# Kernel optimization log

Measured on AMD Instinct MI355X. Metric: run time of the kernel, lower is better.

The kernel has to match this reference:

```python
import jax, jax.numpy as jnp
import numpy as np

EMBED_DIM = 512
NUM_HEADS = 8
HEAD_DIM = EMBED_DIM // NUM_HEADS
LN_EPS = 1e-5


def setup_inputs() -> dict:
    key = jax.random.key(0)
    ks = jax.random.split(key, 7)
    B, S, E = 2, 4096, EMBED_DIM
    s = 1.0 / np.sqrt(E)
    return {
        "x": jax.random.normal(ks[0], (B, S, E), dtype=jnp.float32),
        "qkv_w": jax.random.normal(ks[1], (E, 3 * E), dtype=jnp.float32) * s,
        "qkv_b": jax.random.normal(ks[2], (3 * E,), dtype=jnp.float32) * 0.01,
        "out_w": jax.random.normal(ks[3], (E, E), dtype=jnp.float32) * s,
        "out_b": jax.random.normal(ks[4], (E,), dtype=jnp.float32) * 0.01,
        "ln_g": jnp.ones((E,), dtype=jnp.float32),
        "ln_b": jnp.zeros((E,), dtype=jnp.float32),
    }


def reference(x, qkv_w, qkv_b, out_w, out_b, ln_g, ln_b):
    B, S, E = x.shape
    H, D = NUM_HEADS, HEAD_DIM
    scale = D ** -0.5
    qkv = x @ qkv_w + qkv_b                     # (B, S, 3E)
    qkv = qkv.reshape(B, S, 3, H, D)
    q, k, v = qkv[:, :, 0], qkv[:, :, 1], qkv[:, :, 2]  # (B, S, H, D)
    scores = jnp.einsum("bshd,bthd->bhst", q, k) * scale  # (B, H, S, S)
    probs = jax.nn.softmax(scores, axis=-1)
    ctx = jnp.einsum("bhst,bthd->bshd", probs, v).reshape(B, S, E)
    out = ctx @ out_w + out_b + x               # residual
    mu = out.mean(-1, keepdims=True)
    var = out.var(-1, keepdims=True)
    return (out - mu) * jax.lax.rsqrt(var + LN_EPS) * ln_g + ln_b
```

## Files before the change

### kernel.cpp

```cpp
#include <hip/hip_runtime.h>
#include <stdint.h>

typedef __bf16 bf16x8 __attribute__((ext_vector_type(8)));
typedef float f32x4 __attribute__((ext_vector_type(4)));
typedef float f32x16 __attribute__((ext_vector_type(16)));
typedef float float4v __attribute__((ext_vector_type(4)));
typedef unsigned short u16x4 __attribute__((ext_vector_type(4)));
typedef unsigned short u16x8 __attribute__((ext_vector_type(8)));
typedef unsigned int u32x4v __attribute__((ext_vector_type(4)));

#define DEVI __device__ __forceinline__

static constexpr int Bv = 2, Sv = 4096, Ev = 512, Hv = 8, Dv = 64;
static constexpr int Mv = Bv * Sv;
static constexpr int N3v = 3 * Ev;
static constexpr float QSCALE = 0.125f * 1.4426950408889634f;
static constexpr float C0 = -8.0f;

#if __has_builtin(__builtin_amdgcn_exp2f)
#define EXP2F(x) __builtin_amdgcn_exp2f(x)
#else
#define EXP2F(x) exp2f(x)
#endif

DEVI unsigned short f2bf(float f) {
    unsigned int u = __builtin_bit_cast(unsigned int, f);
    u += 0x7fffu + ((u >> 16) & 1u);
    return (unsigned short)(u >> 16);
}

DEVI float b2f(unsigned short u) {
    return __builtin_bit_cast(float, (unsigned int)u << 16);
}

DEVI unsigned int cvtpk(float lo, float hi) {
    unsigned int r;
    asm("v_cvt_pk_bf16_f32 %0, %1, %2" : "=v"(r) : "v"(lo), "v"(hi));
    return r;
}

DEVI void gload16(const void* src, void* lds) {
    __builtin_amdgcn_global_load_lds(
        (const __attribute__((address_space(1))) unsigned int*)src,
        (__attribute__((address_space(3))) unsigned int*)lds,
        16, 0, 0);
}

__global__ __launch_bounds__(256) void k_convert(const float* __restrict__ in,
                                                 unsigned short* __restrict__ out, int n4) {
    int i = blockIdx.x * 256 + threadIdx.x;
    int stride = gridDim.x * 256;
    for (; i < n4; i += stride) {
        float4v v = ((const float4v*)in)[i];
        u16x4 o;
        o[0] = f2bf(v[0]); o[1] = f2bf(v[1]); o[2] = f2bf(v[2]); o[3] = f2bf(v[3]);
        ((u16x4*)out)[i] = o;
    }
}

__global__ __launch_bounds__(256) void k_tconv(const float* __restrict__ in,
                                               unsigned short* __restrict__ out, int K, int N) {
    __shared__ float lds[32][36];
    int tilesN = N >> 5;
    int tn = blockIdx.x % tilesN, tk = blockIdx.x / tilesN;
    int k0 = tk << 5, n0 = tn << 5;
    int t = threadIdx.x;
    int r = t >> 3, c4 = (t & 7) << 2;
    float4v v = *(const float4v*)(in + (size_t)(k0 + r) * N + n0 + c4);
    *(float4v*)&lds[r][c4] = v;
    __syncthreads();
    int nn = t >> 3, kc = (t & 7) << 2;
    u16x4 o;
#pragma unroll
    for (int j = 0; j < 4; ++j) o[j] = f2bf(lds[kc + j][nn]);
    *(u16x4*)(out + (size_t)(n0 + nn) * K + k0 + kc) = o;
}

template <int EPI>
__global__ __launch_bounds__(256) void k_gemm(
    const unsigned short* __restrict__ A, const unsigned short* __restrict__ Bt,
    int M, int N, int K, const float* __restrict__ bias,
    unsigned short* __restrict__ Qb, unsigned short* __restrict__ Kb,
    unsigned short* __restrict__ Vtb,
    const float* __restrict__ xres, float* __restrict__ outf) {
    __shared__ char smem[32768];
    char* As = smem;
    char* Bs = smem + 16384;
    int nbt = N >> 7;
    int mb = blockIdx.x / nbt, nbi = blockIdx.x % nbt;
    int m0 = mb << 7, n0 = nbi << 7;
    int tid = threadIdx.x, lane = tid & 63, wave = tid >> 6;
    int wr = wave >> 1, wc = wave & 1;

    f32x4 acc[4][4];
    f32x4 zero = {0.f, 0.f, 0.f, 0.f};
#pragma unroll
    for (int a = 0; a < 4; ++a)
#pragma unroll
        for (int b = 0; b < 4; ++b) acc[a][b] = zero;

    for (int kt = 0; kt < K; kt += 64) {
        __syncthreads();
#pragma unroll
        for (int j = 0; j < 4; ++j) {
            int la = (((wave << 2) + j) << 10) + lane * 16;
            int r = la >> 7, cb = la & 127;
            int cbs = cb ^ ((r & 7) << 4);
            gload16((const char*)(A + (size_t)(m0 + r) * K + kt) + cbs,
                    As + (((wave << 2) + j) << 10));
            gload16((const char*)(Bt + (size_t)(n0 + r) * K + kt) + cbs,
                    Bs + (((wave << 2) + j) << 10));
        }
        asm volatile("s_waitcnt vmcnt(0)" ::: "memory");
        __syncthreads();

        bf16x8 af[4][2], bfr[4][2];
#pragma unroll
        for (int rf = 0; rf < 4; ++rf)
#pragma unroll
            for (int c = 0; c < 2; ++c) {
                int row = (wr << 6) + (rf << 4) + (lane & 15);
                int col = (c << 6) + ((lane >> 4) << 4);
                af[rf][c] = *(const bf16x8*)(As + row * 128 + (col ^ ((row & 7) << 4)));
                int rowb = (wc << 6) + (rf << 4) + (lane & 15);
                bfr[rf][c] = *(const bf16x8*)(Bs + rowb * 128 + (col ^ ((rowb & 7) << 4)));
            }
#pragma unroll
        for (int rf = 0; rf < 4; ++rf)
#pragma unroll
            for (int nf = 0; nf < 4; ++nf)
#pragma unroll
                for (int c = 0; c < 2; ++c)
                    acc[rf][nf] = __builtin_amdgcn_mfma_f32_16x16x32_bf16(
                        af[rf][c], bfr[nf][c], acc[rf][nf], 0, 0, 0);
    }

#pragma unroll
    for (int rf = 0; rf < 4; ++rf)
#pragma unroll
        for (int nf = 0; nf < 4; ++nf) {
            int row0 = m0 + (wr << 6) + (rf << 4) + ((lane >> 4) << 2);
            int col = n0 + (wc << 6) + (nf << 4) + (lane & 15);
            float bv = bias[col];
            if (EPI == 0) {
                int reg = col >> 9, hd = col & 511;
                int h = hd >> 6, d = hd & 63;
                int b = row0 >> 12, s0 = row0 & 4095;
                if (reg == 2) {
                    u16x4 o4;
#pragma unroll
                    for (int i = 0; i < 4; ++i) o4[i] = f2bf(acc[rf][nf][i] + bv);
                    *(u16x4*)(Vtb + ((size_t)((b << 3) + h) * 64 + d) * 4096 + s0) = o4;
                } else {
#pragma unroll
                    for (int i = 0; i < 4; ++i) {
                        float v = acc[rf][nf][i] + bv;
                        size_t idx = ((size_t)((b << 3) + h) * Sv + s0 + i) * Dv + d;
                        if (reg == 0) Qb[idx] = f2bf(v * QSCALE);
                        else          Kb[idx] = f2bf(v);
                    }
                }
            } else {
#pragma unroll
                for (int i = 0; i < 4; ++i) {
                    int row = row0 + i;
                    float v = acc[rf][nf][i] + bv + xres[(size_t)row * N + col];
                    outf[(size_t)row * N + col] = v;
                }
            }
        }
}

__global__ __launch_bounds__(256) void k_attn(const unsigned short* __restrict__ Qb,
                                              const unsigned short* __restrict__ Kb,
                                              const unsigned short* __restrict__ Vtb,
                                              unsigned short* __restrict__ po,
                                              float* __restrict__ pl) {
    __shared__ char smem[32768];
    int bid = blockIdx.x;
    int wg = ((bid & 7) << 7) + (bid >> 3);
    int half = wg & 1, qblk = (wg >> 1) & 31, bh = wg >> 6;
    int tid = threadIdx.x, lane = tid & 63, wave = tid >> 6;
    int l31 = lane & 31, hh = lane >> 5;
    int qrow = (qblk << 7) + (wave << 5) + l31;
    int kvbase = half << 11;

    const unsigned short* Kbase = Kb + (size_t)bh * Sv * Dv + (size_t)kvbase * Dv;
    const unsigned short* Vtbase = Vtb + (size_t)bh * Dv * Sv + kvbase;

    bf16x8 qf[4];
#pragma unroll
    for (int tp = 0; tp < 4; ++tp)
        qf[tp] = *(const bf16x8*)(Qb + ((size_t)bh * Sv + qrow) * Dv + (tp << 4) + (hh << 3));

    const char* src[4];
    int strd[4];
    int ldsoff[4];
#pragma unroll
    for (int j = 0; j < 4; ++j) {
        int off = ((wave << 2) + j) << 10;
        int loff = off + lane * 16;
        ldsoff[j] = off;
        if (off < 8192) {
            int r = loff >> 7, cb = loff & 127;
            src[j] = (const char*)(Kbase + (size_t)r * Dv) + (cb ^ ((r & 7) << 4));
            strd[j] = 64 * Dv * 2;
        } else {
            int lo2 = loff - 8192;
            int r = lo2 >> 7, cb = lo2 & 127;
            src[j] = (const char*)(Vtbase + (size_t)r * Sv) + (cb ^ ((r & 7) << 4));
            strd[j] = 64 * 2;
        }
    }

    int koff[2][4], voff[2][2][2];
#pragma unroll
    for (int c = 0; c < 2; ++c) {
        int krow = (c << 5) + l31;
        int ksw = (krow & 7) << 4;
#pragma unroll
        for (int tp = 0; tp < 4; ++tp)
            koff[c][tp] = krow * 128 + (((tp << 5) + (hh << 4)) ^ ksw);
#pragma unroll
        for (int tl = 0; tl < 2; ++tl) {
            int vcb = (c << 6) + (tl << 5) + (hh << 4);
#pragma unroll
            for (int dt = 0; dt < 2; ++dt) {
                int vrow = (dt << 5) + l31;
                voff[c][tl][dt] = vrow * 128 + (vcb ^ ((vrow & 7) << 4));
            }
        }
    }

    f32x16 o[2];
#pragma unroll
    for (int dt = 0; dt < 2; ++dt)
#pragma unroll
        for (int r = 0; r < 16; ++r) o[dt][r] = 0.f;
    float lsum = 0.f;

#pragma unroll
    for (int j = 0; j < 4; ++j) gload16(src[j], smem + ldsoff[j]);
    __syncthreads();

    for (int kt = 0; kt < 32; ++kt) {
        if (kt < 31) {
            int nb = (kt + 1) & 1;
#pragma unroll
            for (int j = 0; j < 4; ++j)
                gload16(src[j] + (size_t)(kt + 1) * strd[j], smem + nb * 16384 + ldsoff[j]);
        }
        char* Ks = smem + (kt & 1) * 16384;
        char* Vs = Ks + 8192;

#pragma unroll
        for (int c = 0; c < 2; ++c) {
            bf16x8 kf[4];
#pragma unroll
            for (int tp = 0; tp < 4; ++tp)
                kf[tp] = *(const bf16x8*)(Ks + koff[c][tp]);
            f32x16 sc;
#pragma unroll
            for (int r = 0; r < 16; ++r) sc[r] = C0;
            __builtin_amdgcn_s_setprio(1);
#pragma unroll
            for (int tp = 0; tp < 4; ++tp)
                sc = __builtin_amdgcn_mfma_f32_32x32x16_bf16(kf[tp], qf[tp], sc, 0, 0, 0);
            __builtin_amdgcn_s_setprio(0);

            float p[16];
#pragma unroll
            for (int r = 0; r < 16; ++r) p[r] = EXP2F(sc[r]);
            float s0 = (p[0] + p[1]) + (p[2] + p[3]);
            float s1 = (p[4] + p[5]) + (p[6] + p[7]);
            float s2 = (p[8] + p[9]) + (p[10] + p[11]);
            float s3 = (p[12] + p[13]) + (p[14] + p[15]);
            lsum += (s0 + s1) + (s2 + s3);

            unsigned int W[8];
#pragma unroll
            for (int i = 0; i < 8; ++i) W[i] = cvtpk(p[2 * i], p[2 * i + 1]);

#pragma unroll
            for (int tl = 0; tl < 2; ++tl) {
                unsigned int a1 = W[4 * tl], b1 = W[4 * tl + 2];
                unsigned int a2 = W[4 * tl + 1], b2 = W[4 * tl + 3];
                asm volatile("v_permlane32_swap_b32 %0, %1" : "+v"(a1), "+v"(b1));
                asm volatile("v_permlane32_swap_b32 %0, %1" : "+v"(a2), "+v"(b2));
                u32x4v uu;
                uu[0] = a1; uu[1] = a2; uu[2] = b1; uu[3] = b2;
                bf16x8 pf = __builtin_bit_cast(bf16x8, uu);
                __builtin_amdgcn_s_setprio(1);
#pragma unroll
                for (int dt = 0; dt < 2; ++dt) {
                    bf16x8 vf = *(const bf16x8*)(Vs + voff[c][tl][dt]);
                    o[dt] = __builtin_amdgcn_mfma_f32_32x32x16_bf16(vf, pf, o[dt], 0, 0, 0);
                }
                __builtin_amdgcn_s_setprio(0);
            }
        }
        __syncthreads();
    }

    lsum += __shfl_xor(lsum, 32, 64);
    if (!hh) pl[((size_t)half * 16 + bh) * Sv + qrow] = lsum;
    size_t obase = (((size_t)half * 16 + bh) * Sv + qrow) * 64;
#pragma unroll
    for (int dt = 0; dt < 2; ++dt)
#pragma unroll
        for (int rp = 0; rp < 8; ++rp) {
            int r = rp << 1;
            int d = (dt << 5) + (r & 3) + ((r >> 2) << 3) + (hh << 2);
            unsigned int w = cvtpk(o[dt][r], o[dt][r + 1]);
            *(unsigned int*)(po + obase + d) = w;
        }
}

__global__ __launch_bounds__(256) void k_merge(const unsigned short* __restrict__ po,
                                               const float* __restrict__ pl,
                                               unsigned short* __restrict__ ctx) {
    int t = blockIdx.x * 256 + threadIdx.x;
    int d8 = t & 7, s = (t >> 3) & 4095, bh = t >> 15;
    int b = bh >> 3, h = bh & 7;
    size_t r0 = ((size_t)bh * 4096 + s) * 64 + (d8 << 3);
    size_t r1 = r0 + (size_t)16 * 4096 * 64;
    u16x8 pa = *(const u16x8*)(po + r0);
    u16x8 pb = *(const u16x8*)(po + r1);
    float inv = 1.f / (pl[(size_t)bh * 4096 + s] + pl[(size_t)16 * 4096 + bh * 4096 + s]);
    u32x4v w;
#pragma unroll
    for (int j = 0; j < 4; ++j) {
        float lo = (b2f(pa[2 * j]) + b2f(pb[2 * j])) * inv;
        float hi = (b2f(pa[2 * j + 1]) + b2f(pb[2 * j + 1])) * inv;
        w[j] = cvtpk(lo, hi);
    }
    *(u32x4v*)(ctx + ((size_t)b * 4096 + s) * 512 + (h << 6) + (d8 << 3)) = w;
}

__global__ __launch_bounds__(256) void k_ln(const float* __restrict__ in,
                                            const float* __restrict__ g,
                                            const float* __restrict__ bta,
                                            float* __restrict__ out) {
    int wave = threadIdx.x >> 6, lane = threadIdx.x & 63;
    size_t row = (size_t)blockIdx.x * 4 + wave;
    const float* p = in + row * 512 + lane * 8;
    float4v v0 = *(const float4v*)p;
    float4v v1 = *(const float4v*)(p + 4);
    float s = 0.f, q = 0.f;
#pragma unroll
    for (int j = 0; j < 4; ++j) {
        s += v0[j] + v1[j];
        q += v0[j] * v0[j] + v1[j] * v1[j];
    }
#pragma unroll
    for (int off = 1; off < 64; off <<= 1) {
        s += __shfl_xor(s, off, 64);
        q += __shfl_xor(q, off, 64);
    }
    float mu = s * (1.f / 512.f);
    float var = q * (1.f / 512.f) - mu * mu;
    float rs = rsqrtf(var + 1e-5f);
    int c = lane * 8;
    float4v o0, o1;
#pragma unroll
    for (int j = 0; j < 4; ++j) {
        o0[j] = (v0[j] - mu) * rs * g[c + j] + bta[c + j];
        o1[j] = (v1[j] - mu) * rs * g[c + 4 + j] + bta[c + 4 + j];
    }
    *(float4v*)(out + row * 512 + c) = o0;
    *(float4v*)(out + row * 512 + c + 4) = o1;
}

extern "C" void kernel_launch(void* const* d_in, const int* in_sizes, int n_in,
                              void* d_out, int out_size, void* d_ws, size_t ws_size,
                              hipStream_t stream) {
    const float* x     = (const float*)d_in[0];
    const float* qkv_w = (const float*)d_in[1];
    const float* qkv_b = (const float*)d_in[2];
    const float* out_w = (const float*)d_in[3];
    const float* out_b = (const float*)d_in[4];
    const float* ln_g  = (const float*)d_in[5];
    const float* ln_b  = (const float*)d_in[6];
    float* out = (float*)d_out;
    char* ws = (char*)d_ws;

    unsigned short* xb    = (unsigned short*)(ws);
    unsigned short* wqkvT = (unsigned short*)(ws + 8388608);
    unsigned short* owT   = (unsigned short*)(ws + 9961472);
    unsigned short* Qb    = (unsigned short*)(ws + 10485760);
    unsigned short* Kb    = (unsigned short*)(ws + 18874368);
    unsigned short* Vtb   = (unsigned short*)(ws + 27262976);
    unsigned short* ctxb  = (unsigned short*)(ws + 35651584);
    unsigned short* po    = (unsigned short*)(ws + 44040192);
    float* tmp            = (float*)(ws + 44040192);
    float* pl             = (float*)(ws + 60817408);

    k_convert<<<2048, 256, 0, stream>>>(x, xb, Mv * Ev / 4);
    k_tconv<<<(512 / 32) * (1536 / 32), 256, 0, stream>>>(qkv_w, wqkvT, 512, 1536);
    k_tconv<<<(512 / 32) * (512 / 32), 256, 0, stream>>>(out_w, owT, 512, 512);
    k_gemm<0><<<(Mv / 128) * (N3v / 128), 256, 0, stream>>>(
        xb, wqkvT, Mv, N3v, Ev, qkv_b, Qb, Kb, Vtb, nullptr, nullptr);
    k_attn<<<1024, 256, 0, stream>>>(Qb, Kb, Vtb, po, pl);
    k_merge<<<2048, 256, 0, stream>>>(po, pl, ctxb);
    k_gemm<1><<<(Mv / 128) * (Ev / 128), 256, 0, stream>>>(
        ctxb, owT, Mv, Ev, Ev, out_b, nullptr, nullptr, nullptr, x, tmp);
    k_ln<<<Mv / 4, 256, 0, stream>>>(tmp, ln_g, ln_b, out);
}
```

Before: 160.8 us.

## Process two query sub-tiles per wave in attention to reuse K/V fragments

Each wave now handles 64 query rows (two 32-row sub-tiles) instead of 32, so every K and V fragment read from LDS feeds twice as many MFMAs. The K/V tile staging cost per query row is halved and the grid is halved to 512 workgroups. In exchange, register pressure roughly doubles for accumulators and Q fragments, which may lower occupancy, and fewer blocks means worse load balance across the 256 CUs.

```diff
diff --git a/kernel.cpp b/kernel.cpp
--- a/kernel.cpp
+++ b/kernel.cpp
@@ -178,20 +178,23 @@
                                               float* __restrict__ pl) {
     __shared__ char smem[32768];
     int bid = blockIdx.x;
-    int wg = ((bid & 7) << 7) + (bid >> 3);
-    int half = wg & 1, qblk = (wg >> 1) & 31, bh = wg >> 6;
+    int wg = ((bid & 7) << 6) + (bid >> 3);
+    int half = wg & 1, qblk = (wg >> 1) & 15, bh = wg >> 5;
     int tid = threadIdx.x, lane = tid & 63, wave = tid >> 6;
     int l31 = lane & 31, hh = lane >> 5;
-    int qrow = (qblk << 7) + (wave << 5) + l31;
+    int qbase = (qblk << 8) + (wave << 6);
     int kvbase = half << 11;
 
     const unsigned short* Kbase = Kb + (size_t)bh * Sv * Dv + (size_t)kvbase * Dv;
     const unsigned short* Vtbase = Vtb + (size_t)bh * Dv * Sv + kvbase;
 
-    bf16x8 qf[4];
-#pragma unroll
-    for (int tp = 0; tp < 4; ++tp)
-        qf[tp] = *(const bf16x8*)(Qb + ((size_t)bh * Sv + qrow) * Dv + (tp << 4) + (hh << 3));
+    bf16x8 qf[2][4];
+#pragma unroll
+    for (int qs = 0; qs < 2; ++qs)
+#pragma unroll
+        for (int tp = 0; tp < 4; ++tp)
+            qf[qs][tp] = *(const bf16x8*)(Qb + ((size_t)bh * Sv + qbase + (qs << 5) + l31) * Dv +
+                                          (tp << 4) + (hh << 3));
 
     const char* src[4];
     int strd[4];
@@ -232,12 +235,14 @@
         }
     }
 
-    f32x16 o[2];
-#pragma unroll
-    for (int dt = 0; dt < 2; ++dt)
-#pragma unroll
-        for (int r = 0; r < 16; ++r) o[dt][r] = 0.f;
-    float lsum = 0.f;
+    f32x16 o[2][2];
+#pragma unroll
+    for (int qs = 0; qs < 2; ++qs)
+#pragma unroll
+        for (int dt = 0; dt < 2; ++dt)
+#pragma unroll
+            for (int r = 0; r < 16; ++r) o[qs][dt][r] = 0.f;
+    float lsum[2] = {0.f, 0.f};
 
 #pragma unroll
     for (int j = 0; j < 4; ++j) gload16(src[j], smem + ldsoff[j]);
@@ -259,61 +264,73 @@
 #pragma unroll
             for (int tp = 0; tp < 4; ++tp)
                 kf[tp] = *(const bf16x8*)(Ks + koff[c][tp]);
-            f32x16 sc;
-#pragma unroll
-            for (int r = 0; r < 16; ++r) sc[r] = C0;
-            __builtin_amdgcn_s_setprio(1);
-#pragma unroll
-            for (int tp = 0; tp < 4; ++tp)
-                sc = __builtin_amdgcn_mfma_f32_32x32x16_bf16(kf[tp], qf[tp], sc, 0, 0, 0);
-            __builtin_amdgcn_s_setprio(0);
-
-            float p[16];
-#pragma unroll
-            for (int r = 0; r < 16; ++r) p[r] = EXP2F(sc[r]);
-            float s0 = (p[0] + p[1]) + (p[2] + p[3]);
-            float s1 = (p[4] + p[5]) + (p[6] + p[7]);
-            float s2 = (p[8] + p[9]) + (p[10] + p[11]);
-            float s3 = (p[12] + p[13]) + (p[14] + p[15]);
-            lsum += (s0 + s1) + (s2 + s3);
-
-            unsigned int W[8];
-#pragma unroll
-            for (int i = 0; i < 8; ++i) W[i] = cvtpk(p[2 * i], p[2 * i + 1]);
-
-#pragma unroll
-            for (int tl = 0; tl < 2; ++tl) {
-                unsigned int a1 = W[4 * tl], b1 = W[4 * tl + 2];
-                unsigned int a2 = W[4 * tl + 1], b2 = W[4 * tl + 3];
-                asm volatile("v_permlane32_swap_b32 %0, %1" : "+v"(a1), "+v"(b1));
-                asm volatile("v_permlane32_swap_b32 %0, %1" : "+v"(a2), "+v"(b2));
-                u32x4v uu;
-                uu[0] = a1; uu[1] = a2; uu[2] = b1; uu[3] = b2;
-                bf16x8 pf = __builtin_bit_cast(bf16x8, uu);
+            bf16x8 vf[2][2];
+#pragma unroll
+            for (int tl = 0; tl < 2; ++tl)
+#pragma unroll
+                for (int dt = 0; dt < 2; ++dt)
+                    vf[tl][dt] = *(const bf16x8*)(Vs + voff[c][tl][dt]);
+
+#pragma unroll
+            for (int qs = 0; qs < 2; ++qs) {
+                f32x16 sc;
+#pragma unroll
+                for (int r = 0; r < 16; ++r) sc[r] = C0;
                 __builtin_amdgcn_s_setprio(1);
 #pragma unroll
-                for (int dt = 0; dt < 2; ++dt) {
-                    bf16x8 vf = *(const bf16x8*)(Vs + voff[c][tl][dt]);
-                    o[dt] = __builtin_amdgcn_mfma_f32_32x32x16_bf16(vf, pf, o[dt], 0, 0, 0);
+                for (int tp = 0; tp < 4; ++tp)
+                    sc = __builtin_amdgcn_mfma_f32_32x32x16_bf16(kf[tp], qf[qs][tp], sc, 0, 0, 0);
+                __builtin_amdgcn_s_setprio(0);
+
+#pragma unroll
+                for (int r = 0; r < 16; ++r) sc[r] = EXP2F(sc[r]);
+                float s0 = (sc[0] + sc[1]) + (sc[2] + sc[3]);
+                float s1 = (sc[4] + sc[5]) + (sc[6] + sc[7]);
+                float s2 = (sc[8] + sc[9]) + (sc[10] + sc[11]);
+                float s3 = (sc[12] + sc[13]) + (sc[14] + sc[15]);
+                lsum[qs] += (s0 + s1) + (s2 + s3);
+
+                unsigned int W[8];
+#pragma unroll
+                for (int i = 0; i < 8; ++i) W[i] = cvtpk(sc[2 * i], sc[2 * i + 1]);
+
+#pragma unroll
+                for (int tl = 0; tl < 2; ++tl) {
+                    unsigned int a1 = W[4 * tl], b1 = W[4 * tl + 2];
+                    unsigned int a2 = W[4 * tl + 1], b2 = W[4 * tl + 3];
+                    asm volatile("v_permlane32_swap_b32 %0, %1" : "+v"(a1), "+v"(b1));
+                    asm volatile("v_permlane32_swap_b32 %0, %1" : "+v"(a2), "+v"(b2));
+                    u32x4v uu;
+                    uu[0] = a1; uu[1] = a2; uu[2] = b1; uu[3] = b2;
+                    bf16x8 pf = __builtin_bit_cast(bf16x8, uu);
+                    __builtin_amdgcn_s_setprio(1);
+#pragma unroll
+                    for (int dt = 0; dt < 2; ++dt)
+                        o[qs][dt] = __builtin_amdgcn_mfma_f32_32x32x16_bf16(vf[tl][dt], pf,
+                                                                            o[qs][dt], 0, 0, 0);
+                    __builtin_amdgcn_s_setprio(0);
                 }
-                __builtin_amdgcn_s_setprio(0);
             }
         }
         __syncthreads();
     }
 
-    lsum += __shfl_xor(lsum, 32, 64);
-    if (!hh) pl[((size_t)half * 16 + bh) * Sv + qrow] = lsum;
-    size_t obase = (((size_t)half * 16 + bh) * Sv + qrow) * 64;
-#pragma unroll
-    for (int dt = 0; dt < 2; ++dt)
-#pragma unroll
-        for (int rp = 0; rp < 8; ++rp) {
-            int r = rp << 1;
-            int d = (dt << 5) + (r & 3) + ((r >> 2) << 3) + (hh << 2);
-            unsigned int w = cvtpk(o[dt][r], o[dt][r + 1]);
-            *(unsigned int*)(po + obase + d) = w;
-        }
+#pragma unroll
+    for (int qs = 0; qs < 2; ++qs) {
+        float ls = lsum[qs] + __shfl_xor(lsum[qs], 32, 64);
+        int qrow = qbase + (qs << 5) + l31;
+        if (!hh) pl[((size_t)half * 16 + bh) * Sv + qrow] = ls;
+        size_t obase = (((size_t)half * 16 + bh) * Sv + qrow) * 64;
+#pragma unroll
+        for (int dt = 0; dt < 2; ++dt)
+#pragma unroll
+            for (int rp = 0; rp < 8; ++rp) {
+                int r = rp << 1;
+                int d = (dt << 5) + (r & 3) + ((r >> 2) << 3) + (hh << 2);
+                unsigned int w = cvtpk(o[qs][dt][r], o[qs][dt][r + 1]);
+                *(unsigned int*)(po + obase + d) = w;
+            }
+    }
 }
 
 __global__ __launch_bounds__(256) void k_merge(const unsigned short* __restrict__ po,
@@ -400,7 +417,7 @@
     k_tconv<<<(512 / 32) * (512 / 32), 256, 0, stream>>>(out_w, owT, 512, 512);
     k_gemm<0><<<(Mv / 128) * (N3v / 128), 256, 0, stream>>>(
         xb, wqkvT, Mv, N3v, Ev, qkv_b, Qb, Kb, Vtb, nullptr, nullptr);
-    k_attn<<<1024, 256, 0, stream>>>(Qb, Kb, Vtb, po, pl);
+    k_attn<<<512, 256, 0, stream>>>(Qb, Kb, Vtb, po, pl);
     k_merge<<<2048, 256, 0, stream>>>(po, pl, ctxb);
     k_gemm<1><<<(Mv / 128) * (Ev / 128), 256, 0, stream>>>(
         ctxb, owT, Mv, Ev, Ev, out_b, nullptr, nullptr, nullptr, x, tmp);
```

After: 174.6 us. +8.6%, slower.

## Restructure attention to 8-wave blocks with triple-buffered 32-key chunks

Applied to the files above, without the earlier changes.

The attention kernel now launches half as many blocks of 512 threads. Each block covers 256 query rows, so every K/V tile loaded into LDS is shared by twice as many waves. The KV loop moves to 32-key chunks held in a three-stage LDS ring, with one 16-byte global load per thread per chunk and a manual vmcnt wait plus barrier in place of double buffering and __syncthreads. All K and V fragments are loaded from LDS before the MFMAs rather than interleaved with them. The workspace layout is also reshuffled so buffers alias one another. The aim is more reuse and deeper prefetch, at the cost of one barrier per smaller chunk and fewer blocks resident per CU.

```diff
diff --git a/kernel.cpp b/kernel.cpp
--- a/kernel.cpp
+++ b/kernel.cpp
@@ -171,66 +171,57 @@
         }
 }
 
-__global__ __launch_bounds__(256) void k_attn(const unsigned short* __restrict__ Qb,
+__global__ __launch_bounds__(512) void k_attn(const unsigned short* __restrict__ Qb,
                                               const unsigned short* __restrict__ Kb,
                                               const unsigned short* __restrict__ Vtb,
                                               unsigned short* __restrict__ po,
                                               float* __restrict__ pl) {
-    __shared__ char smem[32768];
+    __shared__ char smem[24576];
     int bid = blockIdx.x;
-    int wg = ((bid & 7) << 7) + (bid >> 3);
-    int half = wg & 1, qblk = (wg >> 1) & 31, bh = wg >> 6;
+    int wg = ((bid & 7) << 6) + (bid >> 3);
+    int half = wg & 1, qblk = (wg >> 1) & 15, bh = wg >> 5;
     int tid = threadIdx.x, lane = tid & 63, wave = tid >> 6;
     int l31 = lane & 31, hh = lane >> 5;
-    int qrow = (qblk << 7) + (wave << 5) + l31;
+    int qrow = (qblk << 8) + (wave << 5) + l31;
     int kvbase = half << 11;
-
-    const unsigned short* Kbase = Kb + (size_t)bh * Sv * Dv + (size_t)kvbase * Dv;
-    const unsigned short* Vtbase = Vtb + (size_t)bh * Dv * Sv + kvbase;
+    const int NCH = 64;
+
+    const char* Kbase = (const char*)(Kb + (size_t)bh * Sv * Dv + (size_t)kvbase * Dv);
+    const char* Vtbase = (const char*)(Vtb + (size_t)bh * Dv * Sv + kvbase);
 
     bf16x8 qf[4];
 #pragma unroll
     for (int tp = 0; tp < 4; ++tp)
         qf[tp] = *(const bf16x8*)(Qb + ((size_t)bh * Sv + qrow) * Dv + (tp << 4) + (hh << 3));
 
-    const char* src[4];
-    int strd[4];
-    int ldsoff[4];
-#pragma unroll
-    for (int j = 0; j < 4; ++j) {
-        int off = ((wave << 2) + j) << 10;
-        int loff = off + lane * 16;
-        ldsoff[j] = off;
-        if (off < 8192) {
-            int r = loff >> 7, cb = loff & 127;
-            src[j] = (const char*)(Kbase + (size_t)r * Dv) + (cb ^ ((r & 7) << 4));
-            strd[j] = 64 * Dv * 2;
+    const char* src0;
+    size_t st0;
+    int d0;
+    {
+        int j = wave;
+        if (j < 4) {
+            int lo = (j << 10) + lane * 16, r = lo >> 7, cb = lo & 127;
+            src0 = Kbase + (size_t)r * 128 + (cb ^ ((r & 7) << 4));
+            st0 = 4096; d0 = j << 10;
         } else {
-            int lo2 = loff - 8192;
-            int r = lo2 >> 7, cb = lo2 & 127;
-            src[j] = (const char*)(Vtbase + (size_t)r * Sv) + (cb ^ ((r & 7) << 4));
-            strd[j] = 64 * 2;
-        }
-    }
-
-    int koff[2][4], voff[2][2][2];
-#pragma unroll
-    for (int c = 0; c < 2; ++c) {
-        int krow = (c << 5) + l31;
-        int ksw = (krow & 7) << 4;
-#pragma unroll
-        for (int tp = 0; tp < 4; ++tp)
-            koff[c][tp] = krow * 128 + (((tp << 5) + (hh << 4)) ^ ksw);
-#pragma unroll
-        for (int tl = 0; tl < 2; ++tl) {
-            int vcb = (c << 6) + (tl << 5) + (hh << 4);
-#pragma unroll
-            for (int dt = 0; dt < 2; ++dt) {
-                int vrow = (dt << 5) + l31;
-                voff[c][tl][dt] = vrow * 128 + (vcb ^ ((vrow & 7) << 4));
-            }
-        }
-    }
+            int lo = ((j - 4) << 10) + lane * 16, r = lo >> 6, cb = lo & 63;
+            src0 = Vtbase + (size_t)r * 8192 + (cb ^ ((r & 6) << 3));
+            st0 = 64; d0 = 4096 + ((j - 4) << 10);
+        }
+    }
+
+    int koff[4], voff[4];
+#pragma unroll
+    for (int tp = 0; tp < 4; ++tp)
+        koff[tp] = l31 * 128 + (((tp << 5) + (hh << 4)) ^ ((l31 & 7) << 4));
+#pragma unroll
+    for (int tl = 0; tl < 2; ++tl)
+#pragma unroll
+        for (int dt = 0; dt < 2; ++dt) {
+            int row = (dt << 5) + l31;
+            int col = (tl << 5) + (hh << 4);
+            voff[tl * 2 + dt] = row * 64 + (col ^ ((row & 6) << 3));
+        }
 
     f32x16 o[2];
 #pragma unroll
@@ -239,71 +230,68 @@
         for (int r = 0; r < 16; ++r) o[dt][r] = 0.f;
     float lsum = 0.f;
 
-#pragma unroll
-    for (int j = 0; j < 4; ++j) gload16(src[j], smem + ldsoff[j]);
-    __syncthreads();
-
-    for (int kt = 0; kt < 32; ++kt) {
-        if (kt < 31) {
-            int nb = (kt + 1) & 1;
-#pragma unroll
-            for (int j = 0; j < 4; ++j)
-                gload16(src[j] + (size_t)(kt + 1) * strd[j], smem + nb * 16384 + ldsoff[j]);
-        }
-        char* Ks = smem + (kt & 1) * 16384;
-        char* Vs = Ks + 8192;
-
-#pragma unroll
-        for (int c = 0; c < 2; ++c) {
-            bf16x8 kf[4];
-#pragma unroll
-            for (int tp = 0; tp < 4; ++tp)
-                kf[tp] = *(const bf16x8*)(Ks + koff[c][tp]);
-            f32x16 sc;
-#pragma unroll
-            for (int r = 0; r < 16; ++r) sc[r] = C0;
+    gload16(src0, smem + d0);
+    gload16(src0 + st0, smem + 8192 + d0);
+
+    for (int kt = 0; kt < NCH; ++kt) {
+        if (kt < NCH - 1)
+            asm volatile("s_waitcnt vmcnt(1)\n\ts_barrier" ::: "memory");
+        else
+            asm volatile("s_waitcnt vmcnt(0)\n\ts_barrier" ::: "memory");
+        if (kt + 2 < NCH) {
+            int tb = (kt + 2) % 3;
+            gload16(src0 + (size_t)(kt + 2) * st0, smem + tb * 8192 + d0);
+        }
+        char* cbuf = smem + (kt % 3) * 8192;
+        char* vb = cbuf + 4096;
+
+        bf16x8 kf[4], vf[4];
+#pragma unroll
+        for (int tp = 0; tp < 4; ++tp) kf[tp] = *(const bf16x8*)(cbuf + koff[tp]);
+#pragma unroll
+        for (int i = 0; i < 4; ++i) vf[i] = *(const bf16x8*)(vb + voff[i]);
+
+        f32x16 sc;
+#pragma unroll
+        for (int r = 0; r < 16; ++r) sc[r] = C0;
+        __builtin_amdgcn_s_setprio(1);
+#pragma unroll
+        for (int tp = 0; tp < 4; ++tp)
+            sc = __builtin_amdgcn_mfma_f32_32x32x16_bf16(kf[tp], qf[tp], sc, 0, 0, 0);
+        __builtin_amdgcn_s_setprio(0);
+
+#pragma unroll
+        for (int r = 0; r < 16; ++r) sc[r] = EXP2F(sc[r]);
+        float s0 = (sc[0] + sc[1]) + (sc[2] + sc[3]);
+        float s1 = (sc[4] + sc[5]) + (sc[6] + sc[7]);
+        float s2 = (sc[8] + sc[9]) + (sc[10] + sc[11]);
+        float s3 = (sc[12] + sc[13]) + (sc[14] + sc[15]);
+        lsum += (s0 + s1) + (s2 + s3);
+
+        unsigned int W[8];
+#pragma unroll
+        for (int i = 0; i < 8; ++i) W[i] = cvtpk(sc[2 * i], sc[2 * i + 1]);
+
+#pragma unroll
+        for (int tl = 0; tl < 2; ++tl) {
+            unsigned int a1 = W[4 * tl], b1 = W[4 * tl + 2];
+            unsigned int a2 = W[4 * tl + 1], b2 = W[4 * tl + 3];
+            asm volatile("v_permlane32_swap_b32 %0, %1" : "+v"(a1), "+v"(b1));
+            asm volatile("v_permlane32_swap_b32 %0, %1" : "+v"(a2), "+v"(b2));
+            u32x4v uu;
+            uu[0] = a1; uu[1] = a2; uu[2] = b1; uu[3] = b2;
+            bf16x8 pf = __builtin_bit_cast(bf16x8, uu);
             __builtin_amdgcn_s_setprio(1);
 #pragma unroll
-            for (int tp = 0; tp < 4; ++tp)
-                sc = __builtin_amdgcn_mfma_f32_32x32x16_bf16(kf[tp], qf[tp], sc, 0, 0, 0);
+            for (int dt = 0; dt < 2; ++dt)
+                o[dt] = __builtin_amdgcn_mfma_f32_32x32x16_bf16(vf[tl * 2 + dt], pf,
+                                                                o[dt], 0, 0, 0);
             __builtin_amdgcn_s_setprio(0);
-
-            float p[16];
-#pragma unroll
-            for (int r = 0; r < 16; ++r) p[r] = EXP2F(sc[r]);
-            float s0 = (p[0] + p[1]) + (p[2] + p[3]);
-            float s1 = (p[4] + p[5]) + (p[6] + p[7]);
-            float s2 = (p[8] + p[9]) + (p[10] + p[11]);
-            float s3 = (p[12] + p[13]) + (p[14] + p[15]);
-            lsum += (s0 + s1) + (s2 + s3);
-
-            unsigned int W[8];
-#pragma unroll
-            for (int i = 0; i < 8; ++i) W[i] = cvtpk(p[2 * i], p[2 * i + 1]);
-
-#pragma unroll
-            for (int tl = 0; tl < 2; ++tl) {
-                unsigned int a1 = W[4 * tl], b1 = W[4 * tl + 2];
-                unsigned int a2 = W[4 * tl + 1], b2 = W[4 * tl + 3];
-                asm volatile("v_permlane32_swap_b32 %0, %1" : "+v"(a1), "+v"(b1));
-                asm volatile("v_permlane32_swap_b32 %0, %1" : "+v"(a2), "+v"(b2));
-                u32x4v uu;
-                uu[0] = a1; uu[1] = a2; uu[2] = b1; uu[3] = b2;
-                bf16x8 pf = __builtin_bit_cast(bf16x8, uu);
-                __builtin_amdgcn_s_setprio(1);
-#pragma unroll
-                for (int dt = 0; dt < 2; ++dt) {
-                    bf16x8 vf = *(const bf16x8*)(Vs + voff[c][tl][dt]);
-                    o[dt] = __builtin_amdgcn_mfma_f32_32x32x16_bf16(vf, pf, o[dt], 0, 0, 0);
-                }
-                __builtin_amdgcn_s_setprio(0);
-            }
-        }
-        __syncthreads();
-    }
-
-    lsum += __shfl_xor(lsum, 32, 64);
-    if (!hh) pl[((size_t)half * 16 + bh) * Sv + qrow] = lsum;
+        }
+    }
+
+    float ls = lsum + __shfl_xor(lsum, 32, 64);
+    if (!hh) pl[((size_t)half * 16 + bh) * Sv + qrow] = ls;
     size_t obase = (((size_t)half * 16 + bh) * Sv + qrow) * 64;
 #pragma unroll
     for (int dt = 0; dt < 2; ++dt)
@@ -384,23 +372,23 @@
     float* out = (float*)d_out;
     char* ws = (char*)d_ws;
 
-    unsigned short* xb    = (unsigned short*)(ws);
-    unsigned short* wqkvT = (unsigned short*)(ws + 8388608);
-    unsigned short* owT   = (unsigned short*)(ws + 9961472);
-    unsigned short* Qb    = (unsigned short*)(ws + 10485760);
-    unsigned short* Kb    = (unsigned short*)(ws + 18874368);
-    unsigned short* Vtb   = (unsigned short*)(ws + 27262976);
-    unsigned short* ctxb  = (unsigned short*)(ws + 35651584);
-    unsigned short* po    = (unsigned short*)(ws + 44040192);
-    float* tmp            = (float*)(ws + 44040192);
+    unsigned short* owT   = (unsigned short*)(ws);
+    unsigned short* wqkvT = (unsigned short*)(ws + 524288);
+    unsigned short* Qb    = (unsigned short*)(ws + 2097152);
+    unsigned short* Kb    = (unsigned short*)(ws + 10485760);
+    unsigned short* Vtb   = (unsigned short*)(ws + 18874368);
+    unsigned short* xb    = (unsigned short*)(ws + 27262976);
+    unsigned short* po    = (unsigned short*)(ws + 27262976);
     float* pl             = (float*)(ws + 60817408);
+    unsigned short* ctxb  = (unsigned short*)(ws + 2097152);
+    float* tmp            = (float*)(ws + 27262976);
 
     k_convert<<<2048, 256, 0, stream>>>(x, xb, Mv * Ev / 4);
     k_tconv<<<(512 / 32) * (1536 / 32), 256, 0, stream>>>(qkv_w, wqkvT, 512, 1536);
     k_tconv<<<(512 / 32) * (512 / 32), 256, 0, stream>>>(out_w, owT, 512, 512);
     k_gemm<0><<<(Mv / 128) * (N3v / 128), 256, 0, stream>>>(
         xb, wqkvT, Mv, N3v, Ev, qkv_b, Qb, Kb, Vtb, nullptr, nullptr);
-    k_attn<<<1024, 256, 0, stream>>>(Qb, Kb, Vtb, po, pl);
+    k_attn<<<512, 512, 0, stream>>>(Qb, Kb, Vtb, po, pl);
     k_merge<<<2048, 256, 0, stream>>>(po, pl, ctxb);
     k_gemm<1><<<(Mv / 128) * (Ev / 128), 256, 0, stream>>>(
         ctxb, owT, Mv, Ev, Ev, out_b, nullptr, nullptr, nullptr, x, tmp);
```

New measurement: 163.6 us. About the same (+1.7%).
